# Optimization experiments

Hardware: AMD Instinct MI355X
Metric: run time of the kernel (lower is better)

## Reference

```python
import jax, jax.numpy as jnp
import numpy as np

D_G, D_2D, D_3D = 512, 768, 1024
D_F, RANK, ATTN_H = 256, 16, 512
B = 8192


def _xavier(key, shape):
    fan_out, fan_in = shape
    lim = float(np.sqrt(6.0 / (fan_in + fan_out)))
    return jax.random.uniform(key, shape, jnp.float32, -lim, lim)


def setup_inputs() -> dict:
    key = jax.random.key(0)
    ks = jax.random.split(key, 12)
    inp = {
        "h_g": jax.random.normal(ks[0], (B, D_G), jnp.float32),
        "h_2d": jax.random.normal(ks[1], (B, D_2D), jnp.float32),
        "h_3d": jax.random.normal(ks[2], (B, D_3D), jnp.float32),
        # modality projections (torch Linear: y = x @ W.T + b)
        "Wg": _xavier(ks[3], (D_F, D_G)),   "bg": jnp.zeros((D_F,), jnp.float32),
        "W2": _xavier(ks[4], (D_F, D_2D)),  "b2": jnp.zeros((D_F,), jnp.float32),
        "W3": _xavier(ks[5], (D_F, D_3D)),  "b3": jnp.zeros((D_F,), jnp.float32),
        # LayerNorm affine params
        "ln_g_w": jnp.ones((D_F,), jnp.float32),  "ln_g_b": jnp.zeros((D_F,), jnp.float32),
        "ln_2_w": jnp.ones((D_F,), jnp.float32),  "ln_2_b": jnp.zeros((D_F,), jnp.float32),
        "ln_3_w": jnp.ones((D_F,), jnp.float32),  "ln_3_b": jnp.zeros((D_F,), jnp.float32),
        # rank expansions (no bias)
        "U": _xavier(ks[6], (RANK * D_F, D_F)),
        "V": _xavier(ks[7], (RANK * D_F, D_F)),
        "S": _xavier(ks[8], (RANK * D_F, D_F)),
        # attention MLP
        "Wa1": _xavier(ks[9], (ATTN_H, D_G + D_2D + D_3D)), "ba1": jnp.zeros((ATTN_H,), jnp.float32),
        "Wa2": _xavier(ks[10], (RANK, ATTN_H)),             "ba2": jnp.zeros((RANK,), jnp.float32),
    }
    return inp


def _layernorm(x, w, b, eps=1e-5):
    mu = jnp.mean(x, axis=-1, keepdims=True)
    var = jnp.var(x, axis=-1, keepdims=True)
    return (x - mu) * jax.lax.rsqrt(var + eps) * w + b


def reference(h_g, h_2d, h_3d, Wg, bg, W2, b2, W3, b3,
              ln_g_w, ln_g_b, ln_2_w, ln_2_b, ln_3_w, ln_3_b,
              U, V, S, Wa1, ba1, Wa2, ba2):
    # proj + LN + ReLU (dropout=0 / eval mode)
    g = jax.nn.relu(_layernorm(h_g @ Wg.T + bg, ln_g_w, ln_g_b))
    d2 = jax.nn.relu(_layernorm(h_2d @ W2.T + b2, ln_2_w, ln_2_b))
    d3 = jax.nn.relu(_layernorm(h_3d @ W3.T + b3, ln_3_w, ln_3_b))
    b = g.shape[0]
    # rank expansion: (B, R, d_f)
    g_r = (g @ U.T).reshape(b, RANK, D_F)
    d2_r = (d2 @ V.T).reshape(b, RANK, D_F)
    d3_r = (d3 @ S.T).reshape(b, RANK, D_F)
    z_r = g_r * d2_r * d3_r  # elementwise tri-linear product
    # rank attention from raw modality concat
    h_cat = jnp.concatenate([h_g, h_2d, h_3d], axis=-1)
    beta = jax.nn.softmax(jax.nn.relu(h_cat @ Wa1.T + ba1) @ Wa2.T + ba2, axis=-1)  # (B, R)
    z = jnp.einsum('brd,br->bd', z_r, beta)  # (B, d_f)
    return z
```

## Files before the change

kernel.cpp:

```cpp
#include <hip/hip_runtime.h>
#include <stdint.h>

#define B_ROWS 8192
#define DG 512
#define D2 768
#define D3 1024
#define DCAT 2304
#define DF 256
#define RANK 16
#define AH 512

#define OFF_WG 0
#define OFF_W2 131072
#define OFF_W3 327680
#define OFF_U  589824
#define OFF_V  1638400
#define OFF_S  2686976
#define OFF_WA1 3735552

#define WS_WBUF  0u
#define WS_HG    9830400u
#define WS_H2    18219008u
#define WS_H3    30801920u
#define WS_GBUF  9830400u
#define WS_PROJ  47579136u
#define WS_A1P   72744960u
#define WS_BETA  89522176u
#define WS_ZPART 47579136u
#define WS_REQUIRED 94240768u

typedef __attribute__((ext_vector_type(8))) short short8;
typedef __attribute__((ext_vector_type(4))) float f32x4;

__device__ inline unsigned short f2bf(float f) {
  union { float f; unsigned int u; } v; v.f = f;
  unsigned int u = v.u + 0x7fffu + ((v.u >> 16) & 1u);
  return (unsigned short)(u >> 16);
}
__device__ inline float bf2f(unsigned short h) {
  union { float f; unsigned int u; } v; v.u = ((unsigned int)h) << 16;
  return v.f;
}

typedef const unsigned int __attribute__((address_space(1)))* as1_u32p;
typedef unsigned int __attribute__((address_space(3)))* as3_u32p;

__device__ inline void g2l16(const unsigned short* g, unsigned short* l) {
  __builtin_amdgcn_global_load_lds((as1_u32p)g, (as3_u32p)l, 16, 0, 0);
}


__global__ __launch_bounds__(256) void cvt_split_k(const float* __restrict__ hg,
                                                   const float* __restrict__ h2,
                                                   const float* __restrict__ h3,
                                                   const float* __restrict__ Wg,
                                                   const float* __restrict__ W2,
                                                   const float* __restrict__ W3,
                                                   const float* __restrict__ U,
                                                   const float* __restrict__ V,
                                                   const float* __restrict__ S,
                                                   const float* __restrict__ Wa1,
                                                   unsigned short* __restrict__ hgb,
                                                   unsigned short* __restrict__ h2b,
                                                   unsigned short* __restrict__ h3b,
                                                   unsigned short* __restrict__ wbuf) {
  const int bid = blockIdx.x;
  const float* src;
  unsigned short* dst;
  int e;
  if (bid < 18432) {
    e = (bid * 256 + threadIdx.x) * 4;
    if (e < 4194304)        { src = hg + e;            dst = hgb + e; }
    else if (e < 10485760)  { src = h2 + (e - 4194304); dst = h2b + (e - 4194304); }
    else                    { src = h3 + (e - 10485760); dst = h3b + (e - 10485760); }
  } else {
    e = ((bid - 18432) * 256 + threadIdx.x) * 4;
    dst = wbuf + e;
    if (e < OFF_W2)       src = Wg  + e;
    else if (e < OFF_W3)  src = W2  + (e - OFF_W2);
    else if (e < OFF_U)   src = W3  + (e - OFF_W3);
    else if (e < OFF_V)   src = U   + (e - OFF_U);
    else if (e < OFF_S)   src = V   + (e - OFF_V);
    else if (e < OFF_WA1) src = S   + (e - OFF_S);
    else                  src = Wa1 + (e - OFF_WA1);
  }
  float4 v = *(const float4*)src;
  ushort4 o;
  o.x = f2bf(v.x); o.y = f2bf(v.y); o.z = f2bf(v.z); o.w = f2bf(v.w);
  *(ushort4*)dst = o;
}


__device__ __forceinline__ void gemm_mainloop_acc(const unsigned short* Ag, int lda,
                                                  const unsigned short* Bg, int ldb,
                                                  int K,
                                                  unsigned short* lA, unsigned short* lB,
                                                  f32x4 acc[4][4]) {
  const int tid = threadIdx.x;
  const int lane = tid & 63;
  const int wr = tid >> 7;
  const int wc = (tid >> 6) & 1;
  const int row_s = tid >> 3;
  const int kc_s = (((tid & 7) ^ ((tid >> 3) & 7)) << 3);
  const int mbase = wr * 64 + (lane & 15);
  const int nbase = wc * 64 + (lane & 15);
  const int kq = lane >> 4;
  const int h = lane & 7;

  const int nsteps = K >> 6;
  for (int ks = 0; ks < nsteps; ++ks) {
    const int k0 = ks << 6;
    __syncthreads();
#pragma unroll
    for (int p = 0; p < 4; ++p) {
      const int row = p * 32 + row_s;
      const int lofs = (p * 256 + tid) * 8;
      g2l16(Ag + (size_t)row * lda + k0 + kc_s, lA + lofs);
      g2l16(Bg + (size_t)row * ldb + k0 + kc_s, lB + lofs);
    }
    __syncthreads();
#pragma unroll
    for (int kk = 0; kk < 2; ++kk) {
      const int kch = (kk << 2) + kq;
      const int ko = ((kch ^ h) << 3);
      short8 af[4], bfr[4];
#pragma unroll
      for (int t = 0; t < 4; ++t) {
        af[t]  = *(const short8*)(lA + (mbase + t * 16) * 64 + ko);
        bfr[t] = *(const short8*)(lB + (nbase + t * 16) * 64 + ko);
      }
#pragma unroll
      for (int ti = 0; ti < 4; ++ti)
#pragma unroll
        for (int tj = 0; tj < 4; ++tj)
          acc[ti][tj] = __builtin_amdgcn_mfma_f32_16x16x32_bf16(af[ti], bfr[tj], acc[ti][tj], 0, 0, 0);
    }
  }
}

__device__ __forceinline__ void zero_acc(f32x4 acc[4][4]) {
#pragma unroll
  for (int i = 0; i < 4; ++i)
#pragma unroll
    for (int j = 0; j < 4; ++j)
      acc[i][j] = (f32x4){0.f, 0.f, 0.f, 0.f};
}


__global__ __launch_bounds__(256) void fatgemm_k(const unsigned short* __restrict__ hgb,
                                                 const unsigned short* __restrict__ h2b,
                                                 const unsigned short* __restrict__ h3b,
                                                 const unsigned short* __restrict__ wbuf,
                                                 float* __restrict__ proj,
                                                 unsigned short* __restrict__ a1part) {
  __shared__ __align__(16) unsigned short lA[128 * 64];
  __shared__ __align__(16) unsigned short lB[128 * 64];
  const int bid = blockIdx.x;
  f32x4 acc[4][4];
  const int lane = threadIdx.x & 63;
  const int wr = threadIdx.x >> 7, wc = (threadIdx.x >> 6) & 1;
  zero_acc(acc);

  if (bid < 384) {
    const int z = bid >> 7;
    const int local = bid & 127;
    const int m0 = (local >> 1) << 7;
    const int n0 = (local & 1) << 7;
    const int Kz   = (z == 0) ? DG : (z == 1 ? D2 : D3);
    const unsigned short* Ab = (z == 0) ? hgb : (z == 1 ? h2b : h3b);
    const int woff = (z == 0) ? OFF_WG : (z == 1 ? OFF_W2 : OFF_W3);
    gemm_mainloop_acc(Ab + (size_t)m0 * Kz, Kz,
                      wbuf + woff + (size_t)n0 * Kz, Kz, Kz, lA, lB, acc);
    float* out = proj + (size_t)z * B_ROWS * DF;
    const int r0 = m0 + wr * 64 + ((lane >> 4) << 2);
    const int c0 = n0 + wc * 64 + (lane & 15);
#pragma unroll
    for (int ti = 0; ti < 4; ++ti)
#pragma unroll
      for (int tj = 0; tj < 4; ++tj)
#pragma unroll
        for (int i = 0; i < 4; ++i)
          out[(size_t)(r0 + ti * 16 + i) * DF + (c0 + tj * 16)] = acc[ti][tj][i];
  } else {
    const int t = bid - 384;
    const int half = t >> 8;
    const int local = t & 255;
    const int m0 = (local >> 2) << 7;
    const int n0 = (local & 3) << 7;
    const unsigned short* Bb = wbuf + OFF_WA1 + (size_t)n0 * DCAT;
    if (half == 0) {
      gemm_mainloop_acc(hgb + (size_t)m0 * DG, DG, Bb, DCAT, DG, lA, lB, acc);
      gemm_mainloop_acc(h2b + (size_t)m0 * D2, D2, Bb + DG, DCAT, D2, lA, lB, acc);
    } else {
      gemm_mainloop_acc(h3b + (size_t)m0 * D3, D3, Bb + DG + D2, DCAT, D3, lA, lB, acc);
    }
    unsigned short* out = a1part + (size_t)half * (B_ROWS * AH);
    const int r0 = m0 + wr * 64 + ((lane >> 4) << 2);
    const int c0 = n0 + wc * 64 + (lane & 15);
#pragma unroll
    for (int ti = 0; ti < 4; ++ti)
#pragma unroll
      for (int tj = 0; tj < 4; ++tj)
#pragma unroll
        for (int i = 0; i < 4; ++i)
          out[(size_t)(r0 + ti * 16 + i) * AH + (c0 + tj * 16)] = f2bf(acc[ti][tj][i]);
  }
}


__global__ __launch_bounds__(256) void rank_fused_k(const unsigned short* __restrict__ gbuf,
                                                    const unsigned short* __restrict__ wbuf,
                                                    const float* __restrict__ beta,
                                                    float* __restrict__ zpart) {
  __shared__ __align__(16) unsigned short lA[2 * 128 * 128];
  __shared__ __align__(16) unsigned short lB[2 * 128 * 128];
  __shared__ float lbeta[4 * 128];
  const int m0 = blockIdx.x * 128;
  const int d0 = blockIdx.y * 128;
  const int rg = blockIdx.z * 4;
  const int tid = threadIdx.x;

  for (int i = tid; i < 512; i += 256) {
    const int rr = i >> 7, row = i & 127;
    lbeta[i] = beta[(size_t)(m0 + row) * RANK + rg + rr];
  }

  const int lane = tid & 63;
  const int wr = tid >> 7, wc = (tid >> 6) & 1;
  const int row_s = tid >> 4;
  const int kc_s = (((tid & 15) ^ ((tid >> 4) & 15)) << 3);
  const int mbase = wr * 64 + (lane & 15);
  const int nbase = wc * 64 + (lane & 15);
  const int kq = lane >> 4;
  const int h = lane & 15;
  const int lr0 = wr * 64 + ((lane >> 4) << 2);

  auto stage = [&](int rr, int zi, int ks, unsigned short* dA, unsigned short* dB) {
    const unsigned short* Ag = gbuf + (size_t)zi * (B_ROWS * DF) + (size_t)m0 * DF + (ks << 7);
    const unsigned short* Bg = wbuf + OFF_U + (size_t)zi * 1048576
                             + (size_t)((rg + rr) * 256 + d0) * DF + (ks << 7);
#pragma unroll
    for (int q = 0; q < 8; ++q) {
      const int row = q * 16 + row_s;
      const int lofs = (q * 256 + tid) * 8;
      g2l16(Ag + (size_t)row * DF + kc_s, dA + lofs);
      g2l16(Bg + (size_t)row * DF + kc_s, dB + lofs);
    }
  };

  f32x4 zacc[4][4], prod[4][4], acc[4][4];
#pragma unroll
  for (int ti = 0; ti < 4; ++ti)
#pragma unroll
    for (int tj = 0; tj < 4; ++tj) {
      zacc[ti][tj] = (f32x4){0.f, 0.f, 0.f, 0.f};
      acc[ti][tj]  = (f32x4){0.f, 0.f, 0.f, 0.f};
    }

  auto compute = [&](const unsigned short* sA, const unsigned short* sB) {
#pragma unroll
    for (int kk = 0; kk < 4; ++kk) {
      const int kch = (kk << 2) + kq;
      const int ko = ((kch ^ h) << 3);
      short8 af[4], bfr[4];
#pragma unroll
      for (int t = 0; t < 4; ++t) {
        af[t]  = *(const short8*)(sA + (mbase + t * 16) * 128 + ko);
        bfr[t] = *(const short8*)(sB + (nbase + t * 16) * 128 + ko);
      }
#pragma unroll
      for (int ti = 0; ti < 4; ++ti)
#pragma unroll
        for (int tj = 0; tj < 4; ++tj)
          acc[ti][tj] = __builtin_amdgcn_mfma_f32_16x16x32_bf16(af[ti], bfr[tj], acc[ti][tj], 0, 0, 0);
    }
  };

  stage(0, 0, 0, lA, lB);
  for (int p = 0; p < 12; ++p) {
    const int rr = p / 3;
    const int zi = p - rr * 3;
    __syncthreads();
    stage(rr, zi, 1, lA + 16384, lB + 16384);
    compute(lA, lB);
    __syncthreads();
    if (p + 1 < 12) {
      const int pn = p + 1;
      const int rrn = pn / 3;
      stage(rrn, pn - rrn * 3, 0, lA, lB);
    }
    compute(lA + 16384, lB + 16384);

    if (zi == 0) {
#pragma unroll
      for (int ti = 0; ti < 4; ++ti)
#pragma unroll
        for (int tj = 0; tj < 4; ++tj)
          prod[ti][tj] = acc[ti][tj];
    } else if (zi == 1) {
#pragma unroll
      for (int ti = 0; ti < 4; ++ti)
#pragma unroll
        for (int tj = 0; tj < 4; ++tj)
          prod[ti][tj] *= acc[ti][tj];
    } else {
#pragma unroll
      for (int ti = 0; ti < 4; ++ti) {
        const float4 b4 = *(const float4*)(lbeta + rr * 128 + lr0 + ti * 16);
        const float bv[4] = {b4.x, b4.y, b4.z, b4.w};
#pragma unroll
        for (int tj = 0; tj < 4; ++tj)
#pragma unroll
          for (int i = 0; i < 4; ++i)
            zacc[ti][tj][i] += prod[ti][tj][i] * acc[ti][tj][i] * bv[i];
      }
    }
#pragma unroll
    for (int ti = 0; ti < 4; ++ti)
#pragma unroll
      for (int tj = 0; tj < 4; ++tj)
        acc[ti][tj] = (f32x4){0.f, 0.f, 0.f, 0.f};
  }

  float* zp = zpart + (size_t)blockIdx.z * (B_ROWS * DF);
  const int c0 = d0 + wc * 64 + (lane & 15);
#pragma unroll
  for (int ti = 0; ti < 4; ++ti)
#pragma unroll
    for (int tj = 0; tj < 4; ++tj)
#pragma unroll
      for (int i = 0; i < 4; ++i)
        zp[(size_t)(m0 + lr0 + ti * 16 + i) * DF + (c0 + tj * 16)] = zacc[ti][tj][i];
}


__global__ __launch_bounds__(256) void zsum_k(const float* __restrict__ zpart,
                                              float* __restrict__ z) {
  const int idx = blockIdx.x * 256 + threadIdx.x;
  const size_t e = (size_t)idx * 4;
  const size_t stride = (size_t)B_ROWS * DF;
  float4 a = *(const float4*)(zpart + e);
  float4 b = *(const float4*)(zpart + stride + e);
  float4 c = *(const float4*)(zpart + 2 * stride + e);
  float4 d = *(const float4*)(zpart + 3 * stride + e);
  float4 o;
  o.x = (a.x + b.x) + (c.x + d.x);
  o.y = (a.y + b.y) + (c.y + d.y);
  o.z = (a.z + b.z) + (c.z + d.z);
  o.w = (a.w + b.w) + (c.w + d.w);
  *(float4*)(z + e) = o;
}


__global__ __launch_bounds__(256) void post_k(const float* __restrict__ proj,
                                              const float* __restrict__ bg, const float* __restrict__ b2, const float* __restrict__ b3,
                                              const float* __restrict__ wg, const float* __restrict__ wbg,
                                              const float* __restrict__ w2, const float* __restrict__ wb2,
                                              const float* __restrict__ w3, const float* __restrict__ wb3,
                                              unsigned short* __restrict__ gout,
                                              const unsigned short* __restrict__ a1part,
                                              const float* __restrict__ ba1,
                                              const float* __restrict__ Wa2,
                                              const float* __restrict__ ba2,
                                              float* __restrict__ beta) {
  const int bid = blockIdx.x;
  if (bid < 6144) {
    const int gid = bid * 4 + (threadIdx.x >> 6);
    const int lane = threadIdx.x & 63;
    const int z = gid >> 13;
    const int row = gid & (B_ROWS - 1);
    const float* bias = z == 0 ? bg : (z == 1 ? b2 : b3);
    const float* lw = z == 0 ? wg : (z == 1 ? w2 : w3);
    const float* lb = z == 0 ? wbg : (z == 1 ? wb2 : wb3);
    const float* x = proj + (size_t)z * B_ROWS * DF + (size_t)row * DF + lane * 4;
    float4 v = *(const float4*)x;
    float4 bb = *(const float4*)(bias + lane * 4);
    v.x += bb.x; v.y += bb.y; v.z += bb.z; v.w += bb.w;
    float s = v.x + v.y + v.z + v.w;
    float q = v.x * v.x + v.y * v.y + v.z * v.z + v.w * v.w;
#pragma unroll
    for (int m = 1; m < 64; m <<= 1) { s += __shfl_xor(s, m, 64); q += __shfl_xor(q, m, 64); }
    const float mean = s * (1.f / DF);
    const float var = q * (1.f / DF) - mean * mean;
    const float rs = rsqrtf(var + 1e-5f);
    float4 w4 = *(const float4*)(lw + lane * 4);
    float4 b4 = *(const float4*)(lb + lane * 4);
    ushort4 o;
    o.x = f2bf(fmaxf((v.x - mean) * rs * w4.x + b4.x, 0.f));
    o.y = f2bf(fmaxf((v.y - mean) * rs * w4.y + b4.y, 0.f));
    o.z = f2bf(fmaxf((v.z - mean) * rs * w4.z + b4.z, 0.f));
    o.w = f2bf(fmaxf((v.w - mean) * rs * w4.w + b4.w, 0.f));
    *(ushort4*)(gout + (size_t)z * B_ROWS * DF + (size_t)row * DF + lane * 4) = o;
  } else {
    __shared__ float lw[RANK * AH];
    for (int i = threadIdx.x; i < RANK * AH / 4; i += 256)
      *(float4*)(lw + i * 4) = *(const float4*)(Wa2 + i * 4);
    __syncthreads();
    const int row = (bid - 6144) * 4 + (threadIdx.x >> 6);
    const int lane = threadIdx.x & 63;
    const unsigned short* h0 = a1part + (size_t)row * AH + lane * 8;
    const unsigned short* h1 = h0 + (size_t)B_ROWS * AH;
    const uint4 p0 = *(const uint4*)h0;
    const uint4 p1 = *(const uint4*)h1;
    const unsigned int u0[4] = {p0.x, p0.y, p0.z, p0.w};
    const unsigned int u1[4] = {p1.x, p1.y, p1.z, p1.w};
    float4 ca = *(const float4*)(ba1 + lane * 8);
    float4 cb = *(const float4*)(ba1 + lane * 8 + 4);
    const float bias[8] = {ca.x, ca.y, ca.z, ca.w, cb.x, cb.y, cb.z, cb.w};
    float av[8];
#pragma unroll
    for (int j = 0; j < 4; ++j) {
      const float s0 = bf2f((unsigned short)(u0[j] & 0xffffu)) + bf2f((unsigned short)(u1[j] & 0xffffu));
      const float s1 = bf2f((unsigned short)(u0[j] >> 16)) + bf2f((unsigned short)(u1[j] >> 16));
      av[2 * j]     = fmaxf(s0 + bias[2 * j], 0.f);
      av[2 * j + 1] = fmaxf(s1 + bias[2 * j + 1], 0.f);
    }
    float lg[RANK];
#pragma unroll
    for (int r = 0; r < RANK; ++r) {
      const float* wrow = lw + r * AH + lane * 8;
      float4 wa = *(const float4*)wrow;
      float4 wb = *(const float4*)(wrow + 4);
      float p = av[0] * wa.x + av[1] * wa.y + av[2] * wa.z + av[3] * wa.w
              + av[4] * wb.x + av[5] * wb.y + av[6] * wb.z + av[7] * wb.w;
#pragma unroll
      for (int m = 1; m < 64; m <<= 1) p += __shfl_xor(p, m, 64);
      lg[r] = p + ba2[r];
    }
    float mx = lg[0];
#pragma unroll
    for (int r = 1; r < RANK; ++r) mx = fmaxf(mx, lg[r]);
    float den = 0.f;
#pragma unroll
    for (int r = 0; r < RANK; ++r) { lg[r] = __expf(lg[r] - mx); den += lg[r]; }
    const float inv = 1.f / den;
    if (lane < RANK) {
      float mine = 0.f;
#pragma unroll
      for (int r = 0; r < RANK; ++r) mine = (lane == r) ? lg[r] : mine;
      beta[(size_t)row * RANK + lane] = mine * inv;
    }
  }
}


extern "C" void kernel_launch(void* const* d_in, const int* in_sizes, int n_in,
                              void* d_out, int out_size, void* d_ws, size_t ws_size,
                              hipStream_t stream) {
  if (ws_size < (size_t)WS_REQUIRED) return;

  const float* h_g   = (const float*)d_in[0];
  const float* h_2d  = (const float*)d_in[1];
  const float* h_3d  = (const float*)d_in[2];
  const float* Wg    = (const float*)d_in[3];
  const float* bg    = (const float*)d_in[4];
  const float* W2    = (const float*)d_in[5];
  const float* b2    = (const float*)d_in[6];
  const float* W3    = (const float*)d_in[7];
  const float* b3    = (const float*)d_in[8];
  const float* ln_g_w = (const float*)d_in[9];
  const float* ln_g_b = (const float*)d_in[10];
  const float* ln_2_w = (const float*)d_in[11];
  const float* ln_2_b = (const float*)d_in[12];
  const float* ln_3_w = (const float*)d_in[13];
  const float* ln_3_b = (const float*)d_in[14];
  const float* U     = (const float*)d_in[15];
  const float* V     = (const float*)d_in[16];
  const float* S     = (const float*)d_in[17];
  const float* Wa1   = (const float*)d_in[18];
  const float* ba1   = (const float*)d_in[19];
  const float* Wa2   = (const float*)d_in[20];
  const float* ba2   = (const float*)d_in[21];

  char* ws = (char*)d_ws;
  unsigned short* wbuf   = (unsigned short*)(ws + WS_WBUF);
  unsigned short* hgb    = (unsigned short*)(ws + WS_HG);
  unsigned short* h2b    = (unsigned short*)(ws + WS_H2);
  unsigned short* h3b    = (unsigned short*)(ws + WS_H3);
  unsigned short* gbuf   = (unsigned short*)(ws + WS_GBUF);
  float*          proj   = (float*)(ws + WS_PROJ);
  unsigned short* a1part = (unsigned short*)(ws + WS_A1P);
  float*          beta   = (float*)(ws + WS_BETA);
  float*          zpart  = (float*)(ws + WS_ZPART);
  float* z = (float*)d_out;

  cvt_split_k<<<dim3(23232), dim3(256), 0, stream>>>(h_g, h_2d, h_3d,
                                                     Wg, W2, W3, U, V, S, Wa1,
                                                     hgb, h2b, h3b, wbuf);
  fatgemm_k<<<dim3(896), dim3(256), 0, stream>>>(hgb, h2b, h3b, wbuf, proj, a1part);
  post_k<<<dim3(8192), dim3(256), 0, stream>>>(proj, bg, b2, b3, ln_g_w, ln_g_b,
                                               ln_2_w, ln_2_b, ln_3_w, ln_3_b, gbuf,
                                               a1part, ba1, Wa2, ba2, beta);
  rank_fused_k<<<dim3(64, 2, 4), dim3(256), 0, stream>>>(gbuf, wbuf, beta, zpart);
  zsum_k<<<dim3(2048), dim3(256), 0, stream>>>(zpart, z);
}
```

Baseline: 323.4 us.

## Fuse bias+LayerNorm+ReLU epilogue into projection GEMM, split beta kernel

Projection GEMM blocks now cover a full 256-wide row tile with two accumulator sets, then apply bias, a row LayerNorm (cross-wave reduction via shared memory) and ReLU, and write bf16 directly. This removes the fp32 intermediate projection buffer and its separate post-processing pass. The attention-softmax part becomes its own small kernel. The trade-off is fewer projection blocks, doubled accumulator registers, and a workspace remap.

```diff
diff --git a/kernel.cpp b/kernel.cpp
--- a/kernel.cpp
+++ b/kernel.cpp
@@ -22,11 +22,10 @@
 #define WS_HG    9830400u
 #define WS_H2    18219008u
 #define WS_H3    30801920u
-#define WS_GBUF  9830400u
-#define WS_PROJ  47579136u
+#define WS_ZPART 9830400u
+#define WS_GBUF  47579136u
 #define WS_A1P   72744960u
 #define WS_BETA  89522176u
-#define WS_ZPART 47579136u
 #define WS_REQUIRED 94240768u
 
 typedef __attribute__((ext_vector_type(8))) short short8;
@@ -151,42 +150,99 @@
                                                  const unsigned short* __restrict__ h2b,
                                                  const unsigned short* __restrict__ h3b,
                                                  const unsigned short* __restrict__ wbuf,
-                                                 float* __restrict__ proj,
+                                                 const float* __restrict__ bg,
+                                                 const float* __restrict__ b2,
+                                                 const float* __restrict__ b3,
+                                                 const float* __restrict__ wg, const float* __restrict__ wbg,
+                                                 const float* __restrict__ w2, const float* __restrict__ wb2,
+                                                 const float* __restrict__ w3, const float* __restrict__ wb3,
+                                                 unsigned short* __restrict__ gbuf,
                                                  unsigned short* __restrict__ a1part) {
   __shared__ __align__(16) unsigned short lA[128 * 64];
   __shared__ __align__(16) unsigned short lB[128 * 64];
+  __shared__ float redsum[2][128];
+  __shared__ float redsq[2][128];
   const int bid = blockIdx.x;
-  f32x4 acc[4][4];
   const int lane = threadIdx.x & 63;
   const int wr = threadIdx.x >> 7, wc = (threadIdx.x >> 6) & 1;
-  zero_acc(acc);
-
-  if (bid < 384) {
-    const int z = bid >> 7;
-    const int local = bid & 127;
-    const int m0 = (local >> 1) << 7;
-    const int n0 = (local & 1) << 7;
+
+  if (bid < 192) {
+    const int z = bid / 64;
+    const int m0 = (bid - z * 64) * 128;
     const int Kz   = (z == 0) ? DG : (z == 1 ? D2 : D3);
     const unsigned short* Ab = (z == 0) ? hgb : (z == 1 ? h2b : h3b);
     const int woff = (z == 0) ? OFF_WG : (z == 1 ? OFF_W2 : OFF_W3);
-    gemm_mainloop_acc(Ab + (size_t)m0 * Kz, Kz,
-                      wbuf + woff + (size_t)n0 * Kz, Kz, Kz, lA, lB, acc);
-    float* out = proj + (size_t)z * B_ROWS * DF;
-    const int r0 = m0 + wr * 64 + ((lane >> 4) << 2);
-    const int c0 = n0 + wc * 64 + (lane & 15);
+    const float* bias = (z == 0) ? bg : (z == 1 ? b2 : b3);
+    const float* lnw  = (z == 0) ? wg : (z == 1 ? w2 : w3);
+    const float* lnb  = (z == 0) ? wbg : (z == 1 ? wb2 : wb3);
+
+    f32x4 acc0[4][4], acc1[4][4];
+    zero_acc(acc0); zero_acc(acc1);
+    gemm_mainloop_acc(Ab + (size_t)m0 * Kz, Kz, wbuf + woff, Kz, Kz, lA, lB, acc0);
+    gemm_mainloop_acc(Ab + (size_t)m0 * Kz, Kz, wbuf + woff + (size_t)128 * Kz, Kz, Kz, lA, lB, acc1);
+
+    const int c0 = wc * 64 + (lane & 15);
+    float bv0[4], bv1[4], wv0[4], wv1[4], ob0[4], ob1[4];
+#pragma unroll
+    for (int tj = 0; tj < 4; ++tj) {
+      const int c = c0 + tj * 16;
+      bv0[tj] = bias[c];      bv1[tj] = bias[c + 128];
+      wv0[tj] = lnw[c];       wv1[tj] = lnw[c + 128];
+      ob0[tj] = lnb[c];       ob1[tj] = lnb[c + 128];
+    }
+
+    const int quad = lane >> 4;
 #pragma unroll
     for (int ti = 0; ti < 4; ++ti)
 #pragma unroll
-      for (int tj = 0; tj < 4; ++tj)
-#pragma unroll
-        for (int i = 0; i < 4; ++i)
-          out[(size_t)(r0 + ti * 16 + i) * DF + (c0 + tj * 16)] = acc[ti][tj][i];
+      for (int i = 0; i < 4; ++i) {
+        float s = 0.f, q = 0.f;
+#pragma unroll
+        for (int tj = 0; tj < 4; ++tj) {
+          float v = acc0[ti][tj][i] + bv0[tj];
+          acc0[ti][tj][i] = v; s += v; q += v * v;
+          float w = acc1[ti][tj][i] + bv1[tj];
+          acc1[ti][tj][i] = w; s += w; q += w * w;
+        }
+#pragma unroll
+        for (int m = 1; m < 16; m <<= 1) { s += __shfl_xor(s, m, 64); q += __shfl_xor(q, m, 64); }
+        if ((lane & 15) == 0) {
+          const int rl = wr * 64 + ti * 16 + quad * 4 + i;
+          redsum[wc][rl] = s;
+          redsq[wc][rl] = q;
+        }
+      }
+    __syncthreads();
+
+    unsigned short* gout = gbuf + (size_t)z * B_ROWS * DF;
+    const float inv = 1.f / 256.f;
+#pragma unroll
+    for (int ti = 0; ti < 4; ++ti)
+#pragma unroll
+      for (int i = 0; i < 4; ++i) {
+        const int rl = wr * 64 + ti * 16 + quad * 4 + i;
+        const float S = redsum[0][rl] + redsum[1][rl];
+        const float Q = redsq[0][rl] + redsq[1][rl];
+        const float mean = S * inv;
+        const float var = Q * inv - mean * mean;
+        const float rs = rsqrtf(var + 1e-5f);
+        unsigned short* orow = gout + (size_t)(m0 + rl) * DF;
+#pragma unroll
+        for (int tj = 0; tj < 4; ++tj) {
+          const float v0 = fmaxf((acc0[ti][tj][i] - mean) * rs * wv0[tj] + ob0[tj], 0.f);
+          const float v1 = fmaxf((acc1[ti][tj][i] - mean) * rs * wv1[tj] + ob1[tj], 0.f);
+          orow[c0 + tj * 16] = f2bf(v0);
+          orow[c0 + tj * 16 + 128] = f2bf(v1);
+        }
+      }
   } else {
-    const int t = bid - 384;
+    const int t = bid - 192;
     const int half = t >> 8;
     const int local = t & 255;
     const int m0 = (local >> 2) << 7;
     const int n0 = (local & 3) << 7;
+    f32x4 acc[4][4];
+    zero_acc(acc);
     const unsigned short* Bb = wbuf + OFF_WA1 + (size_t)n0 * DCAT;
     if (half == 0) {
       gemm_mainloop_acc(hgb + (size_t)m0 * DG, DG, Bb, DCAT, DG, lA, lB, acc);
@@ -352,94 +408,58 @@
 }
 
 
-__global__ __launch_bounds__(256) void post_k(const float* __restrict__ proj,
-                                              const float* __restrict__ bg, const float* __restrict__ b2, const float* __restrict__ b3,
-                                              const float* __restrict__ wg, const float* __restrict__ wbg,
-                                              const float* __restrict__ w2, const float* __restrict__ wb2,
-                                              const float* __restrict__ w3, const float* __restrict__ wb3,
-                                              unsigned short* __restrict__ gout,
-                                              const unsigned short* __restrict__ a1part,
+__global__ __launch_bounds__(256) void beta_k(const unsigned short* __restrict__ a1part,
                                               const float* __restrict__ ba1,
                                               const float* __restrict__ Wa2,
                                               const float* __restrict__ ba2,
                                               float* __restrict__ beta) {
-  const int bid = blockIdx.x;
-  if (bid < 6144) {
-    const int gid = bid * 4 + (threadIdx.x >> 6);
-    const int lane = threadIdx.x & 63;
-    const int z = gid >> 13;
-    const int row = gid & (B_ROWS - 1);
-    const float* bias = z == 0 ? bg : (z == 1 ? b2 : b3);
-    const float* lw = z == 0 ? wg : (z == 1 ? w2 : w3);
-    const float* lb = z == 0 ? wbg : (z == 1 ? wb2 : wb3);
-    const float* x = proj + (size_t)z * B_ROWS * DF + (size_t)row * DF + lane * 4;
-    float4 v = *(const float4*)x;
-    float4 bb = *(const float4*)(bias + lane * 4);
-    v.x += bb.x; v.y += bb.y; v.z += bb.z; v.w += bb.w;
-    float s = v.x + v.y + v.z + v.w;
-    float q = v.x * v.x + v.y * v.y + v.z * v.z + v.w * v.w;
-#pragma unroll
-    for (int m = 1; m < 64; m <<= 1) { s += __shfl_xor(s, m, 64); q += __shfl_xor(q, m, 64); }
-    const float mean = s * (1.f / DF);
-    const float var = q * (1.f / DF) - mean * mean;
-    const float rs = rsqrtf(var + 1e-5f);
-    float4 w4 = *(const float4*)(lw + lane * 4);
-    float4 b4 = *(const float4*)(lb + lane * 4);
-    ushort4 o;
-    o.x = f2bf(fmaxf((v.x - mean) * rs * w4.x + b4.x, 0.f));
-    o.y = f2bf(fmaxf((v.y - mean) * rs * w4.y + b4.y, 0.f));
-    o.z = f2bf(fmaxf((v.z - mean) * rs * w4.z + b4.z, 0.f));
-    o.w = f2bf(fmaxf((v.w - mean) * rs * w4.w + b4.w, 0.f));
-    *(ushort4*)(gout + (size_t)z * B_ROWS * DF + (size_t)row * DF + lane * 4) = o;
-  } else {
-    __shared__ float lw[RANK * AH];
-    for (int i = threadIdx.x; i < RANK * AH / 4; i += 256)
-      *(float4*)(lw + i * 4) = *(const float4*)(Wa2 + i * 4);
-    __syncthreads();
-    const int row = (bid - 6144) * 4 + (threadIdx.x >> 6);
-    const int lane = threadIdx.x & 63;
-    const unsigned short* h0 = a1part + (size_t)row * AH + lane * 8;
-    const unsigned short* h1 = h0 + (size_t)B_ROWS * AH;
-    const uint4 p0 = *(const uint4*)h0;
-    const uint4 p1 = *(const uint4*)h1;
-    const unsigned int u0[4] = {p0.x, p0.y, p0.z, p0.w};
-    const unsigned int u1[4] = {p1.x, p1.y, p1.z, p1.w};
-    float4 ca = *(const float4*)(ba1 + lane * 8);
-    float4 cb = *(const float4*)(ba1 + lane * 8 + 4);
-    const float bias[8] = {ca.x, ca.y, ca.z, ca.w, cb.x, cb.y, cb.z, cb.w};
-    float av[8];
-#pragma unroll
-    for (int j = 0; j < 4; ++j) {
-      const float s0 = bf2f((unsigned short)(u0[j] & 0xffffu)) + bf2f((unsigned short)(u1[j] & 0xffffu));
-      const float s1 = bf2f((unsigned short)(u0[j] >> 16)) + bf2f((unsigned short)(u1[j] >> 16));
-      av[2 * j]     = fmaxf(s0 + bias[2 * j], 0.f);
-      av[2 * j + 1] = fmaxf(s1 + bias[2 * j + 1], 0.f);
-    }
-    float lg[RANK];
-#pragma unroll
-    for (int r = 0; r < RANK; ++r) {
-      const float* wrow = lw + r * AH + lane * 8;
-      float4 wa = *(const float4*)wrow;
-      float4 wb = *(const float4*)(wrow + 4);
-      float p = av[0] * wa.x + av[1] * wa.y + av[2] * wa.z + av[3] * wa.w
-              + av[4] * wb.x + av[5] * wb.y + av[6] * wb.z + av[7] * wb.w;
-#pragma unroll
-      for (int m = 1; m < 64; m <<= 1) p += __shfl_xor(p, m, 64);
-      lg[r] = p + ba2[r];
-    }
-    float mx = lg[0];
-#pragma unroll
-    for (int r = 1; r < RANK; ++r) mx = fmaxf(mx, lg[r]);
-    float den = 0.f;
-#pragma unroll
-    for (int r = 0; r < RANK; ++r) { lg[r] = __expf(lg[r] - mx); den += lg[r]; }
-    const float inv = 1.f / den;
-    if (lane < RANK) {
-      float mine = 0.f;
-#pragma unroll
-      for (int r = 0; r < RANK; ++r) mine = (lane == r) ? lg[r] : mine;
-      beta[(size_t)row * RANK + lane] = mine * inv;
-    }
+  __shared__ float lw[RANK * AH];
+  for (int i = threadIdx.x; i < RANK * AH / 4; i += 256)
+    *(float4*)(lw + i * 4) = *(const float4*)(Wa2 + i * 4);
+  __syncthreads();
+  const int row = blockIdx.x * 4 + (threadIdx.x >> 6);
+  const int lane = threadIdx.x & 63;
+  const unsigned short* h0 = a1part + (size_t)row * AH + lane * 8;
+  const unsigned short* h1 = h0 + (size_t)B_ROWS * AH;
+  const uint4 p0 = *(const uint4*)h0;
+  const uint4 p1 = *(const uint4*)h1;
+  const unsigned int u0[4] = {p0.x, p0.y, p0.z, p0.w};
+  const unsigned int u1[4] = {p1.x, p1.y, p1.z, p1.w};
+  float4 ca = *(const float4*)(ba1 + lane * 8);
+  float4 cb = *(const float4*)(ba1 + lane * 8 + 4);
+  const float bias[8] = {ca.x, ca.y, ca.z, ca.w, cb.x, cb.y, cb.z, cb.w};
+  float av[8];
+#pragma unroll
+  for (int j = 0; j < 4; ++j) {
+    const float s0 = bf2f((unsigned short)(u0[j] & 0xffffu)) + bf2f((unsigned short)(u1[j] & 0xffffu));
+    const float s1 = bf2f((unsigned short)(u0[j] >> 16)) + bf2f((unsigned short)(u1[j] >> 16));
+    av[2 * j]     = fmaxf(s0 + bias[2 * j], 0.f);
+    av[2 * j + 1] = fmaxf(s1 + bias[2 * j + 1], 0.f);
+  }
+  float lg[RANK];
+#pragma unroll
+  for (int r = 0; r < RANK; ++r) {
+    const float* wrow = lw + r * AH + lane * 8;
+    float4 wa = *(const float4*)wrow;
+    float4 wb = *(const float4*)(wrow + 4);
+    float p = av[0] * wa.x + av[1] * wa.y + av[2] * wa.z + av[3] * wa.w
+            + av[4] * wb.x + av[5] * wb.y + av[6] * wb.z + av[7] * wb.w;
+#pragma unroll
+    for (int m = 1; m < 64; m <<= 1) p += __shfl_xor(p, m, 64);
+    lg[r] = p + ba2[r];
+  }
+  float mx = lg[0];
+#pragma unroll
+  for (int r = 1; r < RANK; ++r) mx = fmaxf(mx, lg[r]);
+  float den = 0.f;
+#pragma unroll
+  for (int r = 0; r < RANK; ++r) { lg[r] = __expf(lg[r] - mx); den += lg[r]; }
+  const float inv = 1.f / den;
+  if (lane < RANK) {
+    float mine = 0.f;
+#pragma unroll
+    for (int r = 0; r < RANK; ++r) mine = (lane == r) ? lg[r] : mine;
+    beta[(size_t)row * RANK + lane] = mine * inv;
   }
 }
 
@@ -477,20 +497,20 @@
   unsigned short* hgb    = (unsigned short*)(ws + WS_HG);
   unsigned short* h2b    = (unsigned short*)(ws + WS_H2);
   unsigned short* h3b    = (unsigned short*)(ws + WS_H3);
+  float*          zpart  = (float*)(ws + WS_ZPART);
   unsigned short* gbuf   = (unsigned short*)(ws + WS_GBUF);
-  float*          proj   = (float*)(ws + WS_PROJ);
   unsigned short* a1part = (unsigned short*)(ws + WS_A1P);
   float*          beta   = (float*)(ws + WS_BETA);
-  float*          zpart  = (float*)(ws + WS_ZPART);
   float* z = (float*)d_out;
 
   cvt_split_k<<<dim3(23232), dim3(256), 0, stream>>>(h_g, h_2d, h_3d,
                                                      Wg, W2, W3, U, V, S, Wa1,
                                                      hgb, h2b, h3b, wbuf);
-  fatgemm_k<<<dim3(896), dim3(256), 0, stream>>>(hgb, h2b, h3b, wbuf, proj, a1part);
-  post_k<<<dim3(8192), dim3(256), 0, stream>>>(proj, bg, b2, b3, ln_g_w, ln_g_b,
-                                               ln_2_w, ln_2_b, ln_3_w, ln_3_b, gbuf,
-                                               a1part, ba1, Wa2, ba2, beta);
+  fatgemm_k<<<dim3(704), dim3(256), 0, stream>>>(hgb, h2b, h3b, wbuf,
+                                                 bg, b2, b3,
+                                                 ln_g_w, ln_g_b, ln_2_w, ln_2_b,
+                                                 ln_3_w, ln_3_b, gbuf, a1part);
+  beta_k<<<dim3(2048), dim3(256), 0, stream>>>(a1part, ba1, Wa2, ba2, beta);
   rank_fused_k<<<dim3(64, 2, 4), dim3(256), 0, stream>>>(gbuf, wbuf, beta, zpart);
   zsum_k<<<dim3(2048), dim3(256), 0, stream>>>(zpart, z);
 }
```

Result: slower. 342.2 us (+5.8%).
